# Performance work log

Measured on AMD Instinct MI355X. Metric: run time of the kernel, lower is better.

Reference implementation:

```python
import jax, jax.numpy as jnp
import numpy as np

B = 2048
NF = 256          # n_feature
IN = NF + 1       # input dim of embedder
EH = 128          # embedder hidden
E = 64            # embedded_dim
H = 64            # lstm_size (== embedded_dim -> simple attention, no projection)
SH = 256          # policy shared hidden
SD = 128          # shared_dim
NA = NF + 1       # n_action
N_SHUFFLE = 4


def setup_inputs() -> dict:
    key = jax.random.key(0)
    ks = jax.random.split(key, 20)
    s = 0.05
    inp = {
        "state": jax.random.normal(ks[0], (B, NF), jnp.float32),
        "acquired": jax.random.randint(ks[1], (B, NF), 0, 2, jnp.int64),
        # embedder MLP: IN -> EH (relu) -> E
        "W_e1": jax.random.normal(ks[2], (IN, EH), jnp.float32) * s,
        "b_e1": jnp.zeros((EH,), jnp.float32),
        "W_e2": jax.random.normal(ks[3], (EH, E), jnp.float32) * s,
        "b_e2": jnp.zeros((E,), jnp.float32),
        # LSTMCell(E, H), gate order i,f,g,o
        "W_ih": jax.random.normal(ks[4], (E, 4 * H), jnp.float32) * s,
        "W_hh": jax.random.normal(ks[5], (H, 4 * H), jnp.float32) * s,
        "b_ih": jnp.zeros((4 * H,), jnp.float32),
        "b_hh": jnp.zeros((4 * H,), jnp.float32),
        # DuelingNet shared MLP: (H+E) -> SH (relu) -> SD
        "W_s1": jax.random.normal(ks[6], (H + E, SH), jnp.float32) * s,
        "b_s1": jnp.zeros((SH,), jnp.float32),
        "W_s2": jax.random.normal(ks[7], (SH, SD), jnp.float32) * s,
        "b_s2": jnp.zeros((SD,), jnp.float32),
        # pi_net: SD -> SD (relu) -> NA
        "W_p1": jax.random.normal(ks[8], (SD, SD), jnp.float32) * s,
        "b_p1": jnp.zeros((SD,), jnp.float32),
        "W_p2": jax.random.normal(ks[9], (SD, NA), jnp.float32) * s,
        "b_p2": jnp.zeros((NA,), jnp.float32),
        # v_net: SD -> SD (relu) -> 1
        "W_v1": jax.random.normal(ks[10], (SD, SD), jnp.float32) * s,
        "b_v1": jnp.zeros((SD,), jnp.float32),
        "W_v2": jax.random.normal(ks[11], (SD, 1), jnp.float32) * s,
        "b_v2": jnp.zeros((1,), jnp.float32),
    }
    return inp


def reference(state, acquired, W_e1, b_e1, W_e2, b_e2, W_ih, W_hh, b_ih, b_hh,
              W_s1, b_s1, W_s2, b_s2, W_p1, b_p1, W_p2, b_p2, W_v1, b_v1, W_v2, b_v2):
    # ---- state2input: sort acquired one-hot ids descending, gather state values ----
    oh = acquired * (jnp.arange(NF, dtype=acquired.dtype) + 1)          # [B,NF]
    order = jnp.argsort(-oh, axis=-1)                                   # descending, stable
    sorted_oh = jnp.take_along_axis(oh, order, axis=-1)
    onehot = jax.nn.one_hot(sorted_oh, NF + 1, dtype=state.dtype)[:, :, 1:]  # [B,NF,NF]
    vals = jnp.take_along_axis(state, order, axis=-1)[..., None]        # [B,NF,1]
    inputs = jnp.concatenate([vals, onehot], axis=-1)                   # [B,NF,NF+1]
    lengths = jnp.sum(acquired, axis=-1)                                # [B]

    # ---- SetEncoder: per-token embedder MLP ----
    hid = jax.nn.relu(inputs @ W_e1 + b_e1)
    emb = hid @ W_e2 + b_e2                                             # [B,NF,E]

    mask = jnp.arange(NF)[None, :] < lengths[:, None]                   # valid positions
    qt = jnp.zeros((state.shape[0], H), state.dtype)
    ct = qt
    NEG = jnp.asarray(-1e9, state.dtype)
    for _ in range(N_SHUFFLE):
        logits = jnp.einsum('ble,be->bl', emb, qt)
        logits = jnp.where(mask, logits, NEG)
        w = jax.nn.softmax(logits, axis=-1)                             # [B,NF]
        attended = jnp.einsum('bl,ble->be', w, emb)                     # [B,E]
        gates = attended @ W_ih + qt @ W_hh + b_ih + b_hh
        i_g, f_g, g_g, o_g = jnp.split(gates, 4, axis=-1)
        ct = jax.nn.sigmoid(f_g) * ct + jax.nn.sigmoid(i_g) * jnp.tanh(g_g)
        qt = jax.nn.sigmoid(o_g) * jnp.tanh(ct)

    encoded = jnp.concatenate([attended, qt], axis=-1)                  # [B,H+E]
    encoded = jnp.where((lengths > 0)[:, None], encoded, jnp.zeros((), state.dtype))

    # ---- DuelingNet ----
    sh = jax.nn.relu(jax.nn.relu(encoded @ W_s1 + b_s1) @ W_s2 + b_s2)
    adv = jax.nn.relu(sh @ W_p1 + b_p1) @ W_p2 + b_p2                   # [B,NA]
    v = jax.nn.relu(sh @ W_v1 + b_v1) @ W_v2 + b_v2                     # [B,1]
    return v + (adv - jnp.mean(adv, axis=1, keepdims=True))
```

## Files before the change

### kernel.cpp

```cpp
#include <hip/hip_runtime.h>
#include <math.h>

namespace {

constexpr int NF   = 256;
constexpr int EH   = 128;
constexpr int E    = 64;
constexpr int H    = 64;
constexpr int SHD  = 256;
constexpr int SD   = 128;
constexpr int NA   = 257;
constexpr int NSHUF = 4;

__device__ __forceinline__ float fsig(float x) {
  return 1.f / (1.f + __expf(-x));
}
__device__ __forceinline__ float ftanh(float x) {
  return 1.f - 2.f / (__expf(2.f * x) + 1.f);
}

__global__ __launch_bounds__(64)
void seqnet(
    const float* __restrict__ state, const int* __restrict__ acquired,
    const float* __restrict__ We1, const float* __restrict__ be1,
    const float* __restrict__ We2, const float* __restrict__ be2,
    const float* __restrict__ Wih, const float* __restrict__ Whh,
    const float* __restrict__ bih, const float* __restrict__ bhh,
    const float* __restrict__ Ws1, const float* __restrict__ bs1,
    const float* __restrict__ Ws2, const float* __restrict__ bs2,
    const float* __restrict__ Wp1, const float* __restrict__ bp1,
    const float* __restrict__ Wp2, const float* __restrict__ bp2,
    const float* __restrict__ Wv1, const float* __restrict__ bv1,
    const float* __restrict__ Wv2, const float* __restrict__ bv2,
    float* __restrict__ out)
{
  const int row = blockIdx.x;
  const int l   = threadIdx.x;
  const int g   = l >> 4;
  const int sub = l & 15;
  const int kbase = sub * 8;

  __shared__ int   id_s[NF];
  __shared__ __align__(16) float val_s[NF];
  __shared__ __align__(16) float w_s[NF];
  __shared__ __align__(16) float rv_s[EH];
  __shared__ __align__(16) float u_s[EH];
  __shared__ __align__(16) float enc_s[EH];
  __shared__ __align__(16) float t1_s[SHD];
  __shared__ __align__(16) float sh_s[SD];
  __shared__ __align__(16) float a1_s[SD];
  __shared__ __align__(16) float v1_s[SD];

  const int* __restrict__ arow = acquired + row * NF;
  #pragma unroll
  for (int j = 0; j < 4; ++j) { id_s[l + 64 * j] = 0; val_s[l + 64 * j] = 0.f; }
  int aiv[4];
  unsigned long long m0, m1, m2, m3;
  aiv[0] = (arow[l]       != 0); m0 = __ballot(aiv[0]);
  aiv[1] = (arow[64 + l]  != 0); m1 = __ballot(aiv[1]);
  aiv[2] = (arow[128 + l] != 0); m2 = __ballot(aiv[2]);
  aiv[3] = (arow[192 + l] != 0); m3 = __ballot(aiv[3]);
  const int pc0 = __popcll(m0), pc1 = __popcll(m1);
  const int pc2 = __popcll(m2), pc3 = __popcll(m3);
  const int L = pc0 + pc1 + pc2 + pc3;
  {
    const int suf1 = pc1 + pc2 + pc3, suf2 = pc2 + pc3, suf3 = pc3;
    if (aiv[0]) { const int r = (int)__popcll((m0 >> l) >> 1) + suf1;
      id_s[r] = l + 1;       val_s[r] = state[row * NF + l]; }
    if (aiv[1]) { const int r = (int)__popcll((m1 >> l) >> 1) + suf2;
      id_s[r] = 64 + l + 1;  val_s[r] = state[row * NF + 64 + l]; }
    if (aiv[2]) { const int r = (int)__popcll((m2 >> l) >> 1) + suf3;
      id_s[r] = 128 + l + 1; val_s[r] = state[row * NF + 128 + l]; }
    if (aiv[3]) { const int r = (int)__popcll((m3 >> l) >> 1);
      id_s[r] = 192 + l + 1; val_s[r] = state[row * NF + 192 + l]; }
  }

  float qt_r = 0.f, ct_r = 0.f;

  const float4 z0 = *(const float4*)(We1 + kbase);
  const float4 z1 = *(const float4*)(We1 + kbase + 4);
  const float4 c0 = *(const float4*)(be1 + kbase);
  const float4 c1 = *(const float4*)(be1 + kbase + 4);

  if (L > 0) {
    const float invL = 1.f / (float)L;
    const int ntok = (L > g) ? ((L - g + 3) >> 2) : 0;
    for (int it = 0; it < NSHUF; ++it) {
      if (it == 0) {
        #pragma unroll
        for (int j = 0; j < 4; ++j) w_s[l + 64 * j] = invL;
      } else {
        {
          const float4* __restrict__ r0 = (const float4*)(We2 + l * E);
          const float4* __restrict__ r1 = (const float4*)(We2 + (64 + l) * E);
          float a0 = 0.f, a1 = 0.f;
          #pragma unroll
          for (int j = 0; j < 16; ++j) {
            const float4 x0 = r0[j], x1 = r1[j];
            float qv;
            qv = __shfl(qt_r, 4 * j);     a0 = fmaf(x0.x, qv, a0); a1 = fmaf(x1.x, qv, a1);
            qv = __shfl(qt_r, 4 * j + 1); a0 = fmaf(x0.y, qv, a0); a1 = fmaf(x1.y, qv, a1);
            qv = __shfl(qt_r, 4 * j + 2); a0 = fmaf(x0.z, qv, a0); a1 = fmaf(x1.z, qv, a1);
            qv = __shfl(qt_r, 4 * j + 3); a0 = fmaf(x0.w, qv, a0); a1 = fmaf(x1.w, qv, a1);
          }
          rv_s[l] = a0; rv_s[64 + l] = a1;
        }
        const float4 ra = *(const float4*)(rv_s + kbase);
        const float4 rb = *(const float4*)(rv_s + kbase + 4);
        for (int i = 0; i < ntok; ++i) {
          const int tok = 4 * i + g;
          const int   idt = id_s[tok];
          const float vt  = val_s[tok];
          const float4* __restrict__ gr = (const float4*)(We1 + idt * EH + kbase);
          const float4 ga = gr[0], gb = gr[1];
          float h, p;
          h = fmaxf(fmaf(vt, z0.x, ga.x) + c0.x, 0.f); p = h * ra.x;
          h = fmaxf(fmaf(vt, z0.y, ga.y) + c0.y, 0.f); p = fmaf(h, ra.y, p);
          h = fmaxf(fmaf(vt, z0.z, ga.z) + c0.z, 0.f); p = fmaf(h, ra.z, p);
          h = fmaxf(fmaf(vt, z0.w, ga.w) + c0.w, 0.f); p = fmaf(h, ra.w, p);
          h = fmaxf(fmaf(vt, z1.x, gb.x) + c1.x, 0.f); p = fmaf(h, rb.x, p);
          h = fmaxf(fmaf(vt, z1.y, gb.y) + c1.y, 0.f); p = fmaf(h, rb.y, p);
          h = fmaxf(fmaf(vt, z1.z, gb.z) + c1.z, 0.f); p = fmaf(h, rb.z, p);
          h = fmaxf(fmaf(vt, z1.w, gb.w) + c1.w, 0.f); p = fmaf(h, rb.w, p);
          p += __shfl_xor(p, 1); p += __shfl_xor(p, 2);
          p += __shfl_xor(p, 4); p += __shfl_xor(p, 8);
          if (sub == 0) w_s[tok] = p;
        }
        float x0 = w_s[l], x1 = w_s[64 + l], x2 = w_s[128 + l], x3 = w_s[192 + l];
        x0 = (l < L)       ? x0 : -1e30f;
        x1 = (64 + l < L)  ? x1 : -1e30f;
        x2 = (128 + l < L) ? x2 : -1e30f;
        x3 = (192 + l < L) ? x3 : -1e30f;
        float mx = fmaxf(fmaxf(x0, x1), fmaxf(x2, x3));
        #pragma unroll
        for (int d = 32; d > 0; d >>= 1) mx = fmaxf(mx, __shfl_xor(mx, d));
        const float e0 = (l < L)       ? __expf(x0 - mx) : 0.f;
        const float e1 = (64 + l < L)  ? __expf(x1 - mx) : 0.f;
        const float e2 = (128 + l < L) ? __expf(x2 - mx) : 0.f;
        const float e3 = (192 + l < L) ? __expf(x3 - mx) : 0.f;
        float s = (e0 + e1) + (e2 + e3);
        #pragma unroll
        for (int d = 32; d > 0; d >>= 1) s += __shfl_xor(s, d);
        const float inv = 1.f / s;
        w_s[l]       = e0 * inv;
        w_s[64 + l]  = e1 * inv;
        w_s[128 + l] = e2 * inv;
        w_s[192 + l] = e3 * inv;
      }

      float4 ua{0, 0, 0, 0}, ub{0, 0, 0, 0};
      for (int i = 0; i < ntok; ++i) {
        const int tok = 4 * i + g;
        const int   idt = id_s[tok];
        const float vt  = val_s[tok];
        const float wt  = w_s[tok];
        const float4* __restrict__ gr = (const float4*)(We1 + idt * EH + kbase);
        const float4 ga = gr[0], gb = gr[1];
        float h;
        h = fmaxf(fmaf(vt, z0.x, ga.x) + c0.x, 0.f); ua.x = fmaf(wt, h, ua.x);
        h = fmaxf(fmaf(vt, z0.y, ga.y) + c0.y, 0.f); ua.y = fmaf(wt, h, ua.y);
        h = fmaxf(fmaf(vt, z0.z, ga.z) + c0.z, 0.f); ua.z = fmaf(wt, h, ua.z);
        h = fmaxf(fmaf(vt, z0.w, ga.w) + c0.w, 0.f); ua.w = fmaf(wt, h, ua.w);
        h = fmaxf(fmaf(vt, z1.x, gb.x) + c1.x, 0.f); ub.x = fmaf(wt, h, ub.x);
        h = fmaxf(fmaf(vt, z1.y, gb.y) + c1.y, 0.f); ub.y = fmaf(wt, h, ub.y);
        h = fmaxf(fmaf(vt, z1.z, gb.z) + c1.z, 0.f); ub.z = fmaf(wt, h, ub.z);
        h = fmaxf(fmaf(vt, z1.w, gb.w) + c1.w, 0.f); ub.w = fmaf(wt, h, ub.w);
      }
      #pragma unroll
      for (int d = 16; d <= 32; d <<= 1) {
        ua.x += __shfl_xor(ua.x, d); ua.y += __shfl_xor(ua.y, d);
        ua.z += __shfl_xor(ua.z, d); ua.w += __shfl_xor(ua.w, d);
        ub.x += __shfl_xor(ub.x, d); ub.y += __shfl_xor(ub.y, d);
        ub.z += __shfl_xor(ub.z, d); ub.w += __shfl_xor(ub.w, d);
      }
      if (l < 16) {
        *(float4*)(u_s + l * 8)     = ua;
        *(float4*)(u_s + l * 8 + 4) = ub;
      }

      {
        float a0 = 0.f, a1 = 0.f, a2 = 0.f, a3 = 0.f;
        #pragma unroll 4
        for (int k = 0; k < EH; k += 4) {
          a0 = fmaf(u_s[k],     We2[(k)     * E + l], a0);
          a1 = fmaf(u_s[k + 1], We2[(k + 1) * E + l], a1);
          a2 = fmaf(u_s[k + 2], We2[(k + 2) * E + l], a2);
          a3 = fmaf(u_s[k + 3], We2[(k + 3) * E + l], a3);
        }
        enc_s[l] = (a0 + a1) + (a2 + a3) + be2[l];
      }

      float gi = 0.f, gf = 0.f, gg = 0.f, go = 0.f;
      #pragma unroll 2
      for (int e = 0; e < E; ++e) {
        const float av = enc_s[e];
        const float* __restrict__ wc = Wih + e * 256;
        gi = fmaf(av, wc[l],       gi);
        gf = fmaf(av, wc[64 + l],  gf);
        gg = fmaf(av, wc[128 + l], gg);
        go = fmaf(av, wc[192 + l], go);
      }
      if (it > 0) {
        #pragma unroll 2
        for (int e = 0; e < E; ++e) {
          const float qv = __shfl(qt_r, e);
          const float* __restrict__ wc = Whh + e * 256;
          gi = fmaf(qv, wc[l],       gi);
          gf = fmaf(qv, wc[64 + l],  gf);
          gg = fmaf(qv, wc[128 + l], gg);
          go = fmaf(qv, wc[192 + l], go);
        }
      }
      gi += bih[l]       + bhh[l];
      gf += bih[64 + l]  + bhh[64 + l];
      gg += bih[128 + l] + bhh[128 + l];
      go += bih[192 + l] + bhh[192 + l];
      ct_r = fsig(gf) * ct_r + fsig(gi) * ftanh(gg);
      qt_r = fsig(go) * ftanh(ct_r);
    }
    enc_s[64 + l] = qt_r;
  } else {
    enc_s[l] = 0.f; enc_s[64 + l] = 0.f;
  }

  {
    float t0 = 0.f, t1 = 0.f, t2 = 0.f, t3 = 0.f;
    #pragma unroll 2
    for (int k = 0; k < EH; ++k) {
      const float ev = enc_s[k];
      const float* __restrict__ wr = Ws1 + k * SHD;
      t0 = fmaf(ev, wr[l],       t0);
      t1 = fmaf(ev, wr[64 + l],  t1);
      t2 = fmaf(ev, wr[128 + l], t2);
      t3 = fmaf(ev, wr[192 + l], t3);
    }
    t1_s[l]       = fmaxf(t0 + bs1[l],       0.f);
    t1_s[64 + l]  = fmaxf(t1 + bs1[64 + l],  0.f);
    t1_s[128 + l] = fmaxf(t2 + bs1[128 + l], 0.f);
    t1_s[192 + l] = fmaxf(t3 + bs1[192 + l], 0.f);
  }
  {
    float s0 = 0.f, s1 = 0.f;
    #pragma unroll 2
    for (int k = 0; k < SHD; ++k) {
      const float tv = t1_s[k];
      s0 = fmaf(tv, Ws2[k * SD + l],      s0);
      s1 = fmaf(tv, Ws2[k * SD + 64 + l], s1);
    }
    sh_s[l]      = fmaxf(s0 + bs2[l],      0.f);
    sh_s[64 + l] = fmaxf(s1 + bs2[64 + l], 0.f);
  }
  {
    float p0 = 0.f, p1 = 0.f, q0 = 0.f, q1 = 0.f;
    #pragma unroll 2
    for (int k = 0; k < SD; ++k) {
      const float sv = sh_s[k];
      p0 = fmaf(sv, Wp1[k * SD + l],      p0);
      p1 = fmaf(sv, Wp1[k * SD + 64 + l], p1);
      q0 = fmaf(sv, Wv1[k * SD + l],      q0);
      q1 = fmaf(sv, Wv1[k * SD + 64 + l], q1);
    }
    a1_s[l]      = fmaxf(p0 + bp1[l],      0.f);
    a1_s[64 + l] = fmaxf(p1 + bp1[64 + l], 0.f);
    v1_s[l]      = fmaxf(q0 + bv1[l],      0.f);
    v1_s[64 + l] = fmaxf(q1 + bv1[64 + l], 0.f);
  }
  float a0 = 0.f, a1 = 0.f, a2 = 0.f, a3 = 0.f;
  #pragma unroll 2
  for (int k = 0; k < SD; ++k) {
    const float av = a1_s[k];
    const float* __restrict__ wr = Wp2 + k * NA;
    a0 = fmaf(av, wr[l],       a0);
    a1 = fmaf(av, wr[64 + l],  a1);
    a2 = fmaf(av, wr[128 + l], a2);
    a3 = fmaf(av, wr[192 + l], a3);
  }
  a0 += bp2[l]; a1 += bp2[64 + l]; a2 += bp2[128 + l]; a3 += bp2[192 + l];
  float c4 = fmaf(a1_s[2 * l], Wp2[(2 * l) * NA + 256],
                  a1_s[2 * l + 1] * Wp2[(2 * l + 1) * NA + 256]);
  #pragma unroll
  for (int d = 32; d > 0; d >>= 1) c4 += __shfl_xor(c4, d);
  const float adv4 = c4 + bp2[256];
  float vv = fmaf(v1_s[l], Wv2[l], v1_s[64 + l] * Wv2[64 + l]);
  #pragma unroll
  for (int d = 32; d > 0; d >>= 1) vv += __shfl_xor(vv, d);
  const float v = vv + bv2[0];
  float ss = (a0 + a1) + (a2 + a3);
  #pragma unroll
  for (int d = 32; d > 0; d >>= 1) ss += __shfl_xor(ss, d);
  const float mean = (ss + adv4) * (1.f / (float)NA);

  const float base = v - mean;
  float* __restrict__ orow = out + row * NA;
  orow[l]       = base + a0;
  orow[64 + l]  = base + a1;
  orow[128 + l] = base + a2;
  orow[192 + l] = base + a3;
  if (l == 0) orow[256] = base + adv4;
}

}

extern "C" void kernel_launch(void* const* d_in, const int* in_sizes, int n_in,
                              void* d_out, int out_size, void* d_ws, size_t ws_size,
                              hipStream_t stream) {
  const float* state    = (const float*)d_in[0];
  const int*   acquired = (const int*)d_in[1];
  const float* We1 = (const float*)d_in[2];
  const float* be1 = (const float*)d_in[3];
  const float* We2 = (const float*)d_in[4];
  const float* be2 = (const float*)d_in[5];
  const float* Wih = (const float*)d_in[6];
  const float* Whh = (const float*)d_in[7];
  const float* bih = (const float*)d_in[8];
  const float* bhh = (const float*)d_in[9];
  const float* Ws1 = (const float*)d_in[10];
  const float* bs1 = (const float*)d_in[11];
  const float* Ws2 = (const float*)d_in[12];
  const float* bs2 = (const float*)d_in[13];
  const float* Wp1 = (const float*)d_in[14];
  const float* bp1 = (const float*)d_in[15];
  const float* Wp2 = (const float*)d_in[16];
  const float* bp2 = (const float*)d_in[17];
  const float* Wv1 = (const float*)d_in[18];
  const float* bv1 = (const float*)d_in[19];
  const float* Wv2 = (const float*)d_in[20];
  const float* bv2 = (const float*)d_in[21];
  float* out = (float*)d_out;

  const int Bn = in_sizes[0] / NF;
  hipLaunchKernelGGL(seqnet, dim3(Bn), dim3(64), 0, stream,
                     state, acquired, We1, be1, We2, be2, Wih, Whh, bih, bhh,
                     Ws1, bs1, Ws2, bs2, Wp1, bp1, Wp2, bp2, Wv1, bv1, Wv2, bv2,
                     out);
}
```

Measured before the change: 173.7 us.

## Split each row across two wavefronts with shared-memory reductions

Moves from one 64-thread wavefront per batch row to a 128-thread block of two wavefronts. Token loops, the LSTM gate matvecs and the MLP head layers are partitioned across both waves, with partial results combined through shared memory and __syncthreads. The aim is to halve the serial per-row latency by raising per-row parallelism, at the price of many added block barriers and shared-memory round trips in place of register shuffles.

```diff
diff --git a/kernel.cpp b/kernel.cpp
--- a/kernel.cpp
+++ b/kernel.cpp
@@ -19,7 +19,7 @@
   return 1.f - 2.f / (__expf(2.f * x) + 1.f);
 }
 
-__global__ __launch_bounds__(64)
+__global__ __launch_bounds__(128, 2)
 void seqnet(
     const float* __restrict__ state, const int* __restrict__ acquired,
     const float* __restrict__ We1, const float* __restrict__ be1,
@@ -35,47 +35,54 @@
     float* __restrict__ out)
 {
   const int row = blockIdx.x;
-  const int l   = threadIdx.x;
-  const int g   = l >> 4;
-  const int sub = l & 15;
+  const int t   = threadIdx.x;
+  const int l   = t & 63;
+  const int wv  = t >> 6;
+  const int gq  = t >> 4;
+  const int sub = t & 15;
   const int kbase = sub * 8;
 
   __shared__ int   id_s[NF];
   __shared__ __align__(16) float val_s[NF];
   __shared__ __align__(16) float w_s[NF];
   __shared__ __align__(16) float rv_s[EH];
-  __shared__ __align__(16) float u_s[EH];
-  __shared__ __align__(16) float enc_s[EH];
+  __shared__ __align__(16) float pu_s[2][EH];
+  __shared__ __align__(16) float red_s[128];
+  __shared__ __align__(16) float att_s[E];
+  __shared__ __align__(16) float qt_s[H];
+  __shared__ __align__(16) float gates_s[256];
   __shared__ __align__(16) float t1_s[SHD];
   __shared__ __align__(16) float sh_s[SD];
   __shared__ __align__(16) float a1_s[SD];
   __shared__ __align__(16) float v1_s[SD];
-
-  const int* __restrict__ arow = acquired + row * NF;
-  #pragma unroll
-  for (int j = 0; j < 4; ++j) { id_s[l + 64 * j] = 0; val_s[l + 64 * j] = 0.f; }
-  int aiv[4];
-  unsigned long long m0, m1, m2, m3;
-  aiv[0] = (arow[l]       != 0); m0 = __ballot(aiv[0]);
-  aiv[1] = (arow[64 + l]  != 0); m1 = __ballot(aiv[1]);
-  aiv[2] = (arow[128 + l] != 0); m2 = __ballot(aiv[2]);
-  aiv[3] = (arow[192 + l] != 0); m3 = __ballot(aiv[3]);
-  const int pc0 = __popcll(m0), pc1 = __popcll(m1);
-  const int pc2 = __popcll(m2), pc3 = __popcll(m3);
-  const int L = pc0 + pc1 + pc2 + pc3;
-  {
+  __shared__ float wred2[2][3];
+  __shared__ int   L_s;
+
+  if (wv == 0) {
+    const int* __restrict__ arow = acquired + row * NF;
+    #pragma unroll
+    for (int j = 0; j < 4; ++j) { id_s[l + 64 * j] = 0; val_s[l + 64 * j] = 0.f; }
+    const int a0v = (arow[l]       != 0); const unsigned long long m0 = __ballot(a0v);
+    const int a1v = (arow[64 + l]  != 0); const unsigned long long m1 = __ballot(a1v);
+    const int a2v = (arow[128 + l] != 0); const unsigned long long m2 = __ballot(a2v);
+    const int a3v = (arow[192 + l] != 0); const unsigned long long m3 = __ballot(a3v);
+    const int pc0 = __popcll(m0), pc1 = __popcll(m1);
+    const int pc2 = __popcll(m2), pc3 = __popcll(m3);
     const int suf1 = pc1 + pc2 + pc3, suf2 = pc2 + pc3, suf3 = pc3;
-    if (aiv[0]) { const int r = (int)__popcll((m0 >> l) >> 1) + suf1;
+    if (a0v) { const int r = (int)__popcll((m0 >> l) >> 1) + suf1;
       id_s[r] = l + 1;       val_s[r] = state[row * NF + l]; }
-    if (aiv[1]) { const int r = (int)__popcll((m1 >> l) >> 1) + suf2;
+    if (a1v) { const int r = (int)__popcll((m1 >> l) >> 1) + suf2;
       id_s[r] = 64 + l + 1;  val_s[r] = state[row * NF + 64 + l]; }
-    if (aiv[2]) { const int r = (int)__popcll((m2 >> l) >> 1) + suf3;
+    if (a2v) { const int r = (int)__popcll((m2 >> l) >> 1) + suf3;
       id_s[r] = 128 + l + 1; val_s[r] = state[row * NF + 128 + l]; }
-    if (aiv[3]) { const int r = (int)__popcll((m3 >> l) >> 1);
+    if (a3v) { const int r = (int)__popcll((m3 >> l) >> 1);
       id_s[r] = 192 + l + 1; val_s[r] = state[row * NF + 192 + l]; }
-  }
-
-  float qt_r = 0.f, ct_r = 0.f;
+    if (l == 0) L_s = pc0 + pc1 + pc2 + pc3;
+  }
+  __syncthreads();
+  const int L = L_s;
+
+  float ct_r = 0.f;
 
   const float4 z0 = *(const float4*)(We1 + kbase);
   const float4 z1 = *(const float4*)(We1 + kbase + 4);
@@ -84,31 +91,30 @@
 
   if (L > 0) {
     const float invL = 1.f / (float)L;
-    const int ntok = (L > g) ? ((L - g + 3) >> 2) : 0;
+    const int ntok = (L > gq) ? ((L - gq + 7) >> 3) : 0;
     for (int it = 0; it < NSHUF; ++it) {
       if (it == 0) {
-        #pragma unroll
-        for (int j = 0; j < 4; ++j) w_s[l + 64 * j] = invL;
+        w_s[t]       = (t < L)       ? invL : 0.f;
+        w_s[128 + t] = (128 + t < L) ? invL : 0.f;
+        __syncthreads();
       } else {
         {
-          const float4* __restrict__ r0 = (const float4*)(We2 + l * E);
-          const float4* __restrict__ r1 = (const float4*)(We2 + (64 + l) * E);
-          float a0 = 0.f, a1 = 0.f;
+          const float4* __restrict__ wr = (const float4*)(We2 + t * E);
+          float x0 = 0.f, x1 = 0.f, x2 = 0.f, x3 = 0.f;
           #pragma unroll
           for (int j = 0; j < 16; ++j) {
-            const float4 x0 = r0[j], x1 = r1[j];
-            float qv;
-            qv = __shfl(qt_r, 4 * j);     a0 = fmaf(x0.x, qv, a0); a1 = fmaf(x1.x, qv, a1);
-            qv = __shfl(qt_r, 4 * j + 1); a0 = fmaf(x0.y, qv, a0); a1 = fmaf(x1.y, qv, a1);
-            qv = __shfl(qt_r, 4 * j + 2); a0 = fmaf(x0.z, qv, a0); a1 = fmaf(x1.z, qv, a1);
-            qv = __shfl(qt_r, 4 * j + 3); a0 = fmaf(x0.w, qv, a0); a1 = fmaf(x1.w, qv, a1);
+            const float4 w4 = wr[j];
+            const float4 q4 = *(const float4*)(qt_s + 4 * j);
+            x0 = fmaf(w4.x, q4.x, x0); x1 = fmaf(w4.y, q4.y, x1);
+            x2 = fmaf(w4.z, q4.z, x2); x3 = fmaf(w4.w, q4.w, x3);
           }
-          rv_s[l] = a0; rv_s[64 + l] = a1;
-        }
+          rv_s[t] = (x0 + x1) + (x2 + x3);
+        }
+        __syncthreads();
         const float4 ra = *(const float4*)(rv_s + kbase);
         const float4 rb = *(const float4*)(rv_s + kbase + 4);
         for (int i = 0; i < ntok; ++i) {
-          const int tok = 4 * i + g;
+          const int tok = 8 * i + gq;
           const int   idt = id_s[tok];
           const float vt  = val_s[tok];
           const float4* __restrict__ gr = (const float4*)(We1 + idt * EH + kbase);
@@ -126,11 +132,11 @@
           p += __shfl_xor(p, 4); p += __shfl_xor(p, 8);
           if (sub == 0) w_s[tok] = p;
         }
-        float x0 = w_s[l], x1 = w_s[64 + l], x2 = w_s[128 + l], x3 = w_s[192 + l];
-        x0 = (l < L)       ? x0 : -1e30f;
-        x1 = (64 + l < L)  ? x1 : -1e30f;
-        x2 = (128 + l < L) ? x2 : -1e30f;
-        x3 = (192 + l < L) ? x3 : -1e30f;
+        __syncthreads();
+        float x0 = (l < L)       ? w_s[l]       : -1e30f;
+        float x1 = (64 + l < L)  ? w_s[64 + l]  : -1e30f;
+        float x2 = (128 + l < L) ? w_s[128 + l] : -1e30f;
+        float x3 = (192 + l < L) ? w_s[192 + l] : -1e30f;
         float mx = fmaxf(fmaxf(x0, x1), fmaxf(x2, x3));
         #pragma unroll
         for (int d = 32; d > 0; d >>= 1) mx = fmaxf(mx, __shfl_xor(mx, d));
@@ -142,15 +148,14 @@
         #pragma unroll
         for (int d = 32; d > 0; d >>= 1) s += __shfl_xor(s, d);
         const float inv = 1.f / s;
-        w_s[l]       = e0 * inv;
-        w_s[64 + l]  = e1 * inv;
-        w_s[128 + l] = e2 * inv;
-        w_s[192 + l] = e3 * inv;
+        if (wv == 0) { w_s[l]      = e0 * inv; w_s[128 + l] = e2 * inv; }
+        else         { w_s[64 + l] = e1 * inv; w_s[192 + l] = e3 * inv; }
+        __syncthreads();
       }
 
       float4 ua{0, 0, 0, 0}, ub{0, 0, 0, 0};
       for (int i = 0; i < ntok; ++i) {
-        const int tok = 4 * i + g;
+        const int tok = 8 * i + gq;
         const int   idt = id_s[tok];
         const float vt  = val_s[tok];
         const float wt  = w_s[tok];
@@ -174,129 +179,140 @@
         ub.z += __shfl_xor(ub.z, d); ub.w += __shfl_xor(ub.w, d);
       }
       if (l < 16) {
-        *(float4*)(u_s + l * 8)     = ua;
-        *(float4*)(u_s + l * 8 + 4) = ub;
-      }
+        *(float4*)(pu_s[wv] + l * 8)     = ua;
+        *(float4*)(pu_s[wv] + l * 8 + 4) = ub;
+      }
+      __syncthreads();
 
       {
-        float a0 = 0.f, a1 = 0.f, a2 = 0.f, a3 = 0.f;
-        #pragma unroll 4
-        for (int k = 0; k < EH; k += 4) {
-          a0 = fmaf(u_s[k],     We2[(k)     * E + l], a0);
-          a1 = fmaf(u_s[k + 1], We2[(k + 1) * E + l], a1);
-          a2 = fmaf(u_s[k + 2], We2[(k + 2) * E + l], a2);
-          a3 = fmaf(u_s[k + 3], We2[(k + 3) * E + l], a3);
-        }
-        enc_s[l] = (a0 + a1) + (a2 + a3) + be2[l];
-      }
-
-      float gi = 0.f, gf = 0.f, gg = 0.f, go = 0.f;
-      #pragma unroll 2
-      for (int e = 0; e < E; ++e) {
-        const float av = enc_s[e];
-        const float* __restrict__ wc = Wih + e * 256;
-        gi = fmaf(av, wc[l],       gi);
-        gf = fmaf(av, wc[64 + l],  gf);
-        gg = fmaf(av, wc[128 + l], gg);
-        go = fmaf(av, wc[192 + l], go);
-      }
-      if (it > 0) {
+        const int c  = l;
+        const int k0 = wv * 64;
+        float b0 = 0.f, b1 = 0.f, b2 = 0.f, b3 = 0.f;
+        #pragma unroll 2
+        for (int k = 0; k < 64; k += 4) {
+          const int kk = k0 + k;
+          const float u0 = pu_s[0][kk]     + pu_s[1][kk];
+          const float u1 = pu_s[0][kk + 1] + pu_s[1][kk + 1];
+          const float u2 = pu_s[0][kk + 2] + pu_s[1][kk + 2];
+          const float u3 = pu_s[0][kk + 3] + pu_s[1][kk + 3];
+          b0 = fmaf(u0, We2[(kk)     * E + c], b0);
+          b1 = fmaf(u1, We2[(kk + 1) * E + c], b1);
+          b2 = fmaf(u2, We2[(kk + 2) * E + c], b2);
+          b3 = fmaf(u3, We2[(kk + 3) * E + c], b3);
+        }
+        red_s[t] = (b0 + b1) + (b2 + b3);
+      }
+      __syncthreads();
+      if (t < 64) att_s[t] = red_s[t] + red_s[64 + t] + be2[t];
+      __syncthreads();
+
+      {
+        float ga_ = 0.f, gb_ = 0.f;
         #pragma unroll 2
         for (int e = 0; e < E; ++e) {
-          const float qv = __shfl(qt_r, e);
-          const float* __restrict__ wc = Whh + e * 256;
-          gi = fmaf(qv, wc[l],       gi);
-          gf = fmaf(qv, wc[64 + l],  gf);
-          gg = fmaf(qv, wc[128 + l], gg);
-          go = fmaf(qv, wc[192 + l], go);
-        }
-      }
-      gi += bih[l]       + bhh[l];
-      gf += bih[64 + l]  + bhh[64 + l];
-      gg += bih[128 + l] + bhh[128 + l];
-      go += bih[192 + l] + bhh[192 + l];
-      ct_r = fsig(gf) * ct_r + fsig(gi) * ftanh(gg);
-      qt_r = fsig(go) * ftanh(ct_r);
-    }
-    enc_s[64 + l] = qt_r;
+          const float av = att_s[e];
+          const float* __restrict__ wc = Wih + e * 256;
+          ga_ = fmaf(av, wc[t],       ga_);
+          gb_ = fmaf(av, wc[128 + t], gb_);
+        }
+        if (it > 0) {
+          #pragma unroll 2
+          for (int e = 0; e < E; ++e) {
+            const float qv = qt_s[e];
+            const float* __restrict__ wc = Whh + e * 256;
+            ga_ = fmaf(qv, wc[t],       ga_);
+            gb_ = fmaf(qv, wc[128 + t], gb_);
+          }
+        }
+        gates_s[t]       = ga_ + bih[t]       + bhh[t];
+        gates_s[128 + t] = gb_ + bih[128 + t] + bhh[128 + t];
+      }
+      __syncthreads();
+      if (t < 64) {
+        const float ig = gates_s[t];
+        const float fg = gates_s[64 + t];
+        const float gg = gates_s[128 + t];
+        const float og = gates_s[192 + t];
+        ct_r = fsig(fg) * ct_r + fsig(ig) * ftanh(gg);
+        qt_s[t] = fsig(og) * ftanh(ct_r);
+      }
+      __syncthreads();
+    }
   } else {
-    enc_s[l] = 0.f; enc_s[64 + l] = 0.f;
+    if (t < 64) { att_s[t] = 0.f; qt_s[t] = 0.f; }
+    __syncthreads();
   }
 
   {
-    float t0 = 0.f, t1 = 0.f, t2 = 0.f, t3 = 0.f;
+    float p0 = 0.f, p1 = 0.f;
     #pragma unroll 2
-    for (int k = 0; k < EH; ++k) {
-      const float ev = enc_s[k];
+    for (int k = 0; k < 64; ++k) {
+      const float ev = att_s[k];
       const float* __restrict__ wr = Ws1 + k * SHD;
-      t0 = fmaf(ev, wr[l],       t0);
-      t1 = fmaf(ev, wr[64 + l],  t1);
-      t2 = fmaf(ev, wr[128 + l], t2);
-      t3 = fmaf(ev, wr[192 + l], t3);
-    }
-    t1_s[l]       = fmaxf(t0 + bs1[l],       0.f);
-    t1_s[64 + l]  = fmaxf(t1 + bs1[64 + l],  0.f);
-    t1_s[128 + l] = fmaxf(t2 + bs1[128 + l], 0.f);
-    t1_s[192 + l] = fmaxf(t3 + bs1[192 + l], 0.f);
-  }
+      p0 = fmaf(ev, wr[t],       p0);
+      p1 = fmaf(ev, wr[128 + t], p1);
+    }
+    #pragma unroll 2
+    for (int k = 0; k < 64; ++k) {
+      const float qv = qt_s[k];
+      const float* __restrict__ wr = Ws1 + (64 + k) * SHD;
+      p0 = fmaf(qv, wr[t],       p0);
+      p1 = fmaf(qv, wr[128 + t], p1);
+    }
+    t1_s[t]       = fmaxf(p0 + bs1[t],       0.f);
+    t1_s[128 + t] = fmaxf(p1 + bs1[128 + t], 0.f);
+  }
+  __syncthreads();
   {
     float s0 = 0.f, s1 = 0.f;
     #pragma unroll 2
-    for (int k = 0; k < SHD; ++k) {
-      const float tv = t1_s[k];
-      s0 = fmaf(tv, Ws2[k * SD + l],      s0);
-      s1 = fmaf(tv, Ws2[k * SD + 64 + l], s1);
-    }
-    sh_s[l]      = fmaxf(s0 + bs2[l],      0.f);
-    sh_s[64 + l] = fmaxf(s1 + bs2[64 + l], 0.f);
-  }
+    for (int k = 0; k < SHD; k += 2) {
+      s0 = fmaf(t1_s[k],     Ws2[(k)     * SD + t], s0);
+      s1 = fmaf(t1_s[k + 1], Ws2[(k + 1) * SD + t], s1);
+    }
+    sh_s[t] = fmaxf(s0 + s1 + bs2[t], 0.f);
+  }
+  __syncthreads();
   {
-    float p0 = 0.f, p1 = 0.f, q0 = 0.f, q1 = 0.f;
+    float p = 0.f, q = 0.f;
     #pragma unroll 2
     for (int k = 0; k < SD; ++k) {
       const float sv = sh_s[k];
-      p0 = fmaf(sv, Wp1[k * SD + l],      p0);
-      p1 = fmaf(sv, Wp1[k * SD + 64 + l], p1);
-      q0 = fmaf(sv, Wv1[k * SD + l],      q0);
-      q1 = fmaf(sv, Wv1[k * SD + 64 + l], q1);
-    }
-    a1_s[l]      = fmaxf(p0 + bp1[l],      0.f);
-    a1_s[64 + l] = fmaxf(p1 + bp1[64 + l], 0.f);
-    v1_s[l]      = fmaxf(q0 + bv1[l],      0.f);
-    v1_s[64 + l] = fmaxf(q1 + bv1[64 + l], 0.f);
-  }
-  float a0 = 0.f, a1 = 0.f, a2 = 0.f, a3 = 0.f;
+      p = fmaf(sv, Wp1[k * SD + t], p);
+      q = fmaf(sv, Wv1[k * SD + t], q);
+    }
+    a1_s[t] = fmaxf(p + bp1[t], 0.f);
+    v1_s[t] = fmaxf(q + bv1[t], 0.f);
+  }
+  __syncthreads();
+  float a0 = 0.f, a1v = 0.f;
   #pragma unroll 2
   for (int k = 0; k < SD; ++k) {
     const float av = a1_s[k];
     const float* __restrict__ wr = Wp2 + k * NA;
-    a0 = fmaf(av, wr[l],       a0);
-    a1 = fmaf(av, wr[64 + l],  a1);
-    a2 = fmaf(av, wr[128 + l], a2);
-    a3 = fmaf(av, wr[192 + l], a3);
-  }
-  a0 += bp2[l]; a1 += bp2[64 + l]; a2 += bp2[128 + l]; a3 += bp2[192 + l];
-  float c4 = fmaf(a1_s[2 * l], Wp2[(2 * l) * NA + 256],
-                  a1_s[2 * l + 1] * Wp2[(2 * l + 1) * NA + 256]);
+    a0  = fmaf(av, wr[t],       a0);
+    a1v = fmaf(av, wr[128 + t], a1v);
+  }
+  a0 += bp2[t]; a1v += bp2[128 + t];
+  float c4 = a1_s[t] * Wp2[t * NA + 256];
+  float vv = v1_s[t] * Wv2[t];
+  float ss = a0 + a1v;
   #pragma unroll
-  for (int d = 32; d > 0; d >>= 1) c4 += __shfl_xor(c4, d);
-  const float adv4 = c4 + bp2[256];
-  float vv = fmaf(v1_s[l], Wv2[l], v1_s[64 + l] * Wv2[64 + l]);
-  #pragma unroll
-  for (int d = 32; d > 0; d >>= 1) vv += __shfl_xor(vv, d);
-  const float v = vv + bv2[0];
-  float ss = (a0 + a1) + (a2 + a3);
-  #pragma unroll
-  for (int d = 32; d > 0; d >>= 1) ss += __shfl_xor(ss, d);
-  const float mean = (ss + adv4) * (1.f / (float)NA);
-
+  for (int d = 32; d > 0; d >>= 1) {
+    c4 += __shfl_xor(c4, d);
+    vv += __shfl_xor(vv, d);
+    ss += __shfl_xor(ss, d);
+  }
+  if (l == 0) { wred2[wv][0] = c4; wred2[wv][1] = vv; wred2[wv][2] = ss; }
+  __syncthreads();
+  const float adv4 = wred2[0][0] + wred2[1][0] + bp2[256];
+  const float v    = wred2[0][1] + wred2[1][1] + bv2[0];
+  const float mean = (wred2[0][2] + wred2[1][2] + adv4) * (1.f / (float)NA);
   const float base = v - mean;
   float* __restrict__ orow = out + row * NA;
-  orow[l]       = base + a0;
-  orow[64 + l]  = base + a1;
-  orow[128 + l] = base + a2;
-  orow[192 + l] = base + a3;
-  if (l == 0) orow[256] = base + adv4;
+  orow[t]       = base + a0;
+  orow[128 + t] = base + a1v;
+  if (t == 0) orow[256] = base + adv4;
 }
 
 }
@@ -329,7 +345,7 @@
   float* out = (float*)d_out;
 
   const int Bn = in_sizes[0] / NF;
-  hipLaunchKernelGGL(seqnet, dim3(Bn), dim3(64), 0, stream,
+  hipLaunchKernelGGL(seqnet, dim3(Bn), dim3(128), 0, stream,
                      state, acquired, We1, be1, We2, be2, Wih, Whh, bih, bhh,
                      Ws1, bs1, Ws2, bs2, Wp1, bp1, Wp2, bp2, Wv1, bv1, Wv2, bv2,
                      out);
```

Result: slower. 218.0 us (+25.5%).
